# Optimization experiments

Hardware: AMD Instinct MI355X
Metric: run time of the kernel (lower is better)

The kernel has to match this reference:

```python
import jax, jax.numpy as jnp
import numpy as np

F_REP = 256
F_BET = 512
N_PER = 6
MAGNITUDE = 0.001


def _glorot(key, shape):
    fan_in = shape[0]
    return jax.random.normal(key, shape, dtype=jnp.float32) / np.sqrt(fan_in)


def setup_inputs() -> dict:
    key = jax.random.key(0)
    ks = jax.random.split(key, 24)
    n_atoms, n_tors = 50000, 300000
    inp = {
        'h': jax.random.normal(ks[0], (n_atoms, F_REP), dtype=jnp.float32),
        'idxs': jax.random.randint(ks[1], (n_tors, 4), 0, n_atoms, dtype=jnp.int64),
        # symmetrizer: skippedLinear(4*rep, bet) + DenseBlock(bet, depth=3)
        'Ws0': _glorot(ks[2], (4 * F_REP, F_BET)), 'bs0': jnp.zeros((F_BET,), jnp.float32),
        'Ws1': _glorot(ks[3], (F_BET, F_BET)), 'bs1': jnp.zeros((F_BET,), jnp.float32),
        'Ws2': _glorot(ks[4], (F_BET, F_BET)), 'bs2': jnp.zeros((F_BET,), jnp.float32),
        'Ws3': _glorot(ks[5], (F_BET, F_BET)), 'bs3': jnp.zeros((F_BET,), jnp.float32),
        # torsion_nn: DenseBlock(bet, depth=2) + Linear(bet, n_periodicity)
        'Wt0': _glorot(ks[6], (F_BET, F_BET)), 'bt0': jnp.zeros((F_BET,), jnp.float32),
        'Wt1': _glorot(ks[7], (F_BET, F_BET)), 'bt1': jnp.zeros((F_BET,), jnp.float32),
        'Wt2': _glorot(ks[8], (F_BET, N_PER)), 'bt2': jnp.zeros((N_PER,), jnp.float32),
        # classification_nn: skippedLinear(bet, bet) + Linear(bet, n_periodicity)
        'Wc0': _glorot(ks[9], (F_BET, F_BET)), 'bc0': jnp.zeros((F_BET,), jnp.float32),
        'Wc1': _glorot(ks[10], (F_BET, N_PER)), 'bc1': jnp.zeros((N_PER,), jnp.float32),
    }
    return inp


def _symmetrizer(x, Ws0, bs0, Ws1, bs1, Ws2, bs2, Ws3, bs3):
    # skippedLinear(4*rep, bet): dims differ -> plain Linear + ELU
    h = jax.nn.elu(x @ Ws0 + bs0)
    # DenseBlock: residual Linear+ELU layers (in==out)
    for W, b in ((Ws1, bs1), (Ws2, bs2), (Ws3, bs3)):
        h = h + jax.nn.elu(h @ W + b)
    return h


def reference(h, idxs, Ws0, bs0, Ws1, bs1, Ws2, bs2, Ws3, bs3,
              Wt0, bt0, Wt1, bt1, Wt2, bt2, Wc0, bc0, Wc1, bc1):
    feats = h[idxs]  # [N, 4, F_REP] gather
    f1, f2, f3, f4 = feats[:, 0], feats[:, 1], feats[:, 2], feats[:, 3]
    x_fwd = jnp.concatenate([f1, f2, f3, f4], axis=-1)  # [N, 4F]
    x_rev = jnp.concatenate([f4, f3, f2, f1], axis=-1)
    sym = (_symmetrizer(x_fwd, Ws0, bs0, Ws1, bs1, Ws2, bs2, Ws3, bs3)
           + _symmetrizer(x_rev, Ws0, bs0, Ws1, bs1, Ws2, bs2, Ws3, bs3))
    # torsion_nn
    t = sym + jax.nn.elu(sym @ Wt0 + bt0)
    t = t + jax.nn.elu(t @ Wt1 + bt1)
    coeffs = t @ Wt2 + bt2  # [N, n_periodicity]
    # classification_nn (skippedLinear with in==out -> residual)
    c = sym + jax.nn.elu(sym @ Wc0 + bc0)
    score = c @ Wc1 + bc1  # [N, n_periodicity]
    gate = jax.nn.sigmoid(score)  # hardness == 1
    k = coeffs * MAGNITUDE * gate
    return jnp.stack([score, k])  # [2, N, n_periodicity]
```

## Files before the change

### kernel.cpp

```cpp
#include <hip/hip_runtime.h>

#define BM 64
#define NTHREADS 512
#define NT2 1024

typedef __attribute__((ext_vector_type(8))) short short8;
typedef __attribute__((ext_vector_type(4))) float f32x4;

__device__ __forceinline__ short f2bf(float f) {
  unsigned u = __builtin_bit_cast(unsigned, f);
  u += 0x7FFFu + ((u >> 16) & 1u);
  return (short)(u >> 16);
}
__device__ __forceinline__ float bf2f(short s) {
  unsigned u = ((unsigned)(unsigned short)s) << 16;
  return __builtin_bit_cast(float, u);
}
__device__ __forceinline__ float elu_f(float v) {
  return v > 0.f ? v : (__expf(v) - 1.f);
}

__global__ __launch_bounds__(256) void pack_w(const float* __restrict__ src,
                                              short* __restrict__ dst,
                                              int K, int N, int rev) {
  int tile = blockIdx.x * 4 + (threadIdx.x >> 6);
  int lane = threadIdx.x & 63;
  int ktiles = K >> 5;
  int tot = (N >> 4) * ktiles;
  if (tile >= tot) return;
  int nt = tile / ktiles, kt = tile - nt * ktiles;
  int col = (nt << 4) + (lane & 15);
  int k0 = (kt << 5) + ((lane >> 4) << 3);
  short8 o;
#pragma unroll
  for (int j = 0; j < 8; ++j) {
    int kr = k0 + j;
    if (rev) kr = ((3 - (kr >> 8)) << 8) | (kr & 255);
    o[j] = f2bf(src[(size_t)kr * N + col]);
  }
  *(short8*)(dst + (size_t)tile * 512 + lane * 8) = o;
}

__device__ __forceinline__ short8 lds_afrag(const char* base, int stride, int rt,
                                            int kt, int lane) {
  int row = rt * 16 + (lane & 15);
  int boff = (kt << 6) + ((lane >> 4) << 4);
  return *(const short8*)(base + row * stride + (boff ^ ((row & 7) << 4)));
}
__device__ __forceinline__ short8 ldg_bfrag(const short* W, int ktiles, int ct,
                                            int kt, int lane) {
  return *(const short8*)(W + ((size_t)(ct * ktiles + kt) << 9) + (lane << 3));
}

__global__ __launch_bounds__(NTHREADS) void atom_pre(const float* __restrict__ h,
                                                     const short* __restrict__ W0f,
                                                     short* __restrict__ p,
                                                     int n_atoms) {
  __shared__ char sh[BM * 512];
  const int tid = threadIdx.x, lane = tid & 63, wv = tid >> 6;
  const int r0 = blockIdx.x * BM;
  for (int i = tid; i < BM * 32; i += NTHREADS) {
    int row = i >> 5, c0 = (i & 31) << 3;
    int ga = r0 + row;
    short8 o;
    if (ga < n_atoms) {
      const float4* s4 = (const float4*)(h + (size_t)ga * 256 + c0);
      float4 v0 = s4[0], v1 = s4[1];
      o[0] = f2bf(v0.x); o[1] = f2bf(v0.y); o[2] = f2bf(v0.z); o[3] = f2bf(v0.w);
      o[4] = f2bf(v1.x); o[5] = f2bf(v1.y); o[6] = f2bf(v1.z); o[7] = f2bf(v1.w);
    } else {
#pragma unroll
      for (int e = 0; e < 8; ++e) o[e] = 0;
    }
    *(short8*)(sh + row * 512 + ((c0 * 2) ^ ((row & 7) << 4))) = o;
  }
  __syncthreads();
#pragma unroll 1
  for (int s = 0; s < 4; ++s) {
    f32x4 acc[4][4];
    const f32x4 z = {0.f, 0.f, 0.f, 0.f};
#pragma unroll
    for (int rt = 0; rt < 4; ++rt)
#pragma unroll
      for (int cf = 0; cf < 4; ++cf) acc[rt][cf] = z;
    for (int kt = 0; kt < 8; ++kt) {
      short8 a[4], b[4];
#pragma unroll
      for (int rt = 0; rt < 4; ++rt) a[rt] = lds_afrag(sh, 512, rt, kt, lane);
#pragma unroll
      for (int cf = 0; cf < 4; ++cf)
        b[cf] = ldg_bfrag(W0f, 32, (wv << 2) + cf, (s << 3) + kt, lane);
#pragma unroll
      for (int rt = 0; rt < 4; ++rt)
#pragma unroll
        for (int cf = 0; cf < 4; ++cf)
          acc[rt][cf] = __builtin_amdgcn_mfma_f32_16x16x32_bf16(a[rt], b[cf], acc[rt][cf], 0, 0, 0);
    }
#pragma unroll
    for (int rt = 0; rt < 4; ++rt)
#pragma unroll
      for (int cf = 0; cf < 4; ++cf) {
        int col = (wv << 6) + (cf << 4) + (lane & 15);
#pragma unroll
        for (int i = 0; i < 4; ++i) {
          int row = rt * 16 + ((lane >> 4) << 2) + i;
          int ga = r0 + row;
          if (ga < n_atoms) p[((size_t)ga * 4 + s) * 512 + col] = f2bf(acc[rt][cf][i]);
        }
      }
  }
}

struct P2 {
  const int* idxs;
  const short* p;
  const short *W1, *W2, *W3, *Wt0, *Wt1, *Wc0;
  const float *bs0, *bs1, *bs2, *bs3, *bt0, *bt1, *bt2, *bc0, *bc1;
  const float *Wt2, *Wc1;
  float* out;
  int n_tors;
};

template <bool SYM>
__device__ __forceinline__ void layer_dual3(char* hf, char* hr,
                                            const short* __restrict__ W,
                                            const float* __restrict__ bias,
                                            int wv, int lane) {
  f32x4 accf[4][2], accr[4][2];
  const f32x4 z = {0.f, 0.f, 0.f, 0.f};
#pragma unroll
  for (int rt = 0; rt < 4; ++rt)
#pragma unroll
    for (int cf = 0; cf < 2; ++cf) { accf[rt][cf] = z; accr[rt][cf] = z; }
  short8 bC[2], bN[2];
#pragma unroll
  for (int cf = 0; cf < 2; ++cf) bC[cf] = ldg_bfrag(W, 16, (wv << 1) + cf, 0, lane);
#pragma unroll 1
  for (int kt = 0; kt < 16; ++kt) {
#pragma unroll
    for (int cf = 0; cf < 2; ++cf)
      bN[cf] = ldg_bfrag(W, 16, (wv << 1) + cf, (kt + 1) & 15, lane);
    short8 af[4], ar[4];
#pragma unroll
    for (int rt = 0; rt < 4; ++rt) {
      af[rt] = lds_afrag(hf, 1024, rt, kt, lane);
      ar[rt] = lds_afrag(hr, 1024, rt, kt, lane);
    }
#pragma unroll
    for (int rt = 0; rt < 4; ++rt)
#pragma unroll
      for (int cf = 0; cf < 2; ++cf) {
        accf[rt][cf] = __builtin_amdgcn_mfma_f32_16x16x32_bf16(af[rt], bC[cf], accf[rt][cf], 0, 0, 0);
        accr[rt][cf] = __builtin_amdgcn_mfma_f32_16x16x32_bf16(ar[rt], bC[cf], accr[rt][cf], 0, 0, 0);
      }
#pragma unroll
    for (int cf = 0; cf < 2; ++cf) bC[cf] = bN[cf];
  }
  float bcol[2];
#pragma unroll
  for (int cf = 0; cf < 2; ++cf) bcol[cf] = bias[(wv << 5) + (cf << 4) + (lane & 15)];
  __syncthreads();
#pragma unroll
  for (int rt = 0; rt < 4; ++rt)
#pragma unroll
    for (int cf = 0; cf < 2; ++cf) {
      int col = (wv << 5) + (cf << 4) + (lane & 15);
#pragma unroll
      for (int i = 0; i < 4; ++i) {
        int row = rt * 16 + ((lane >> 4) << 2) + i;
        size_t off = (size_t)row * 1024 + ((col * 2) ^ ((row & 7) << 4));
        short* pf = (short*)(hf + off);
        short* pr = (short*)(hr + off);
        float nf = bf2f(*pf) + elu_f(accf[rt][cf][i] + bcol[cf]);
        float nr = bf2f(*pr) + elu_f(accr[rt][cf][i] + bcol[cf]);
        if (SYM) {
          *pf = f2bf(nf + nr);
        } else {
          *pf = f2bf(nf);
          *pr = f2bf(nr);
        }
      }
    }
  __syncthreads();
}

__device__ __forceinline__ void layer_single3(const char* in,
                                              const short* __restrict__ W,
                                              const float* __restrict__ bias,
                                              const char* res, char* out,
                                              int wv, int lane) {
  f32x4 acc[4][2];
  const f32x4 z = {0.f, 0.f, 0.f, 0.f};
#pragma unroll
  for (int rt = 0; rt < 4; ++rt)
#pragma unroll
    for (int cf = 0; cf < 2; ++cf) acc[rt][cf] = z;
  short8 bC[2], bN[2];
#pragma unroll
  for (int cf = 0; cf < 2; ++cf) bC[cf] = ldg_bfrag(W, 16, (wv << 1) + cf, 0, lane);
#pragma unroll 1
  for (int kt = 0; kt < 16; ++kt) {
#pragma unroll
    for (int cf = 0; cf < 2; ++cf)
      bN[cf] = ldg_bfrag(W, 16, (wv << 1) + cf, (kt + 1) & 15, lane);
    short8 a[4];
#pragma unroll
    for (int rt = 0; rt < 4; ++rt) a[rt] = lds_afrag(in, 1024, rt, kt, lane);
#pragma unroll
    for (int rt = 0; rt < 4; ++rt)
#pragma unroll
      for (int cf = 0; cf < 2; ++cf)
        acc[rt][cf] = __builtin_amdgcn_mfma_f32_16x16x32_bf16(a[rt], bC[cf], acc[rt][cf], 0, 0, 0);
#pragma unroll
    for (int cf = 0; cf < 2; ++cf) bC[cf] = bN[cf];
  }
  float bcol[2];
#pragma unroll
  for (int cf = 0; cf < 2; ++cf) bcol[cf] = bias[(wv << 5) + (cf << 4) + (lane & 15)];
  __syncthreads();
#pragma unroll
  for (int rt = 0; rt < 4; ++rt)
#pragma unroll
    for (int cf = 0; cf < 2; ++cf) {
      int col = (wv << 5) + (cf << 4) + (lane & 15);
#pragma unroll
      for (int i = 0; i < 4; ++i) {
        int row = rt * 16 + ((lane >> 4) << 2) + i;
        size_t off = (size_t)row * 1024 + ((col * 2) ^ ((row & 7) << 4));
        float v = elu_f(acc[rt][cf][i] + bcol[cf]) + bf2f(*(const short*)(res + off));
        *(short*)(out + off) = f2bf(v);
      }
    }
  __syncthreads();
}

__global__ __launch_bounds__(NT2) void fused2(P2 p) {
  __shared__ char smem[BM * 2048];
  __shared__ int sIdx[BM * 4];
  __shared__ float sSmall[BM * 12];
  char* sA = smem;
  char* sB = smem + BM * 1024;
  const int tid = threadIdx.x;
  const int lane = tid & 63;
  const int wv = tid >> 6;
  const int r0 = blockIdx.x * BM;

  for (int i = tid; i < BM * 4; i += NT2) {
    int grow = r0 + (i >> 2);
    sIdx[i] = (grow < p.n_tors) ? p.idxs[(size_t)grow * 4 + (i & 3)] : 0;
  }
  __syncthreads();

  for (int i = tid; i < BM * 64; i += NT2) {
    int row = i >> 6, c0 = (i & 63) << 3;
    float sf[8], sr[8];
#pragma unroll
    for (int e = 0; e < 8; ++e) { sf[e] = p.bs0[c0 + e]; sr[e] = sf[e]; }
#pragma unroll
    for (int j = 0; j < 4; ++j) {
      int a = sIdx[row * 4 + j];
      short8 vf = *(const short8*)(p.p + ((size_t)a * 4 + j) * 512 + c0);
      short8 vr = *(const short8*)(p.p + ((size_t)a * 4 + (3 - j)) * 512 + c0);
#pragma unroll
      for (int e = 0; e < 8; ++e) { sf[e] += bf2f(vf[e]); sr[e] += bf2f(vr[e]); }
    }
    short8 of, orv;
#pragma unroll
    for (int e = 0; e < 8; ++e) { of[e] = f2bf(elu_f(sf[e])); orv[e] = f2bf(elu_f(sr[e])); }
    size_t off = (size_t)row * 1024 + ((c0 * 2) ^ ((row & 7) << 4));
    *(short8*)(sA + off) = of;
    *(short8*)(sB + off) = orv;
  }
  __syncthreads();

  layer_dual3<false>(sA, sB, p.W1, p.bs1, wv, lane);
  layer_dual3<false>(sA, sB, p.W2, p.bs2, wv, lane);
  layer_dual3<true >(sA, sB, p.W3, p.bs3, wv, lane);

  layer_single3(sA, p.Wt0, p.bt0, sA, sB, wv, lane);
  layer_single3(sB, p.Wt1, p.bt1, sB, sB, wv, lane);
  layer_single3(sA, p.Wc0, p.bc0, sA, sA, wv, lane);

  for (int idx = tid; idx < BM * 12; idx += NT2) {
    int row = idx / 12, jj = idx - row * 12;
    int j = (jj < 6) ? jj : jj - 6;
    const char* src = (jj < 6) ? sB : sA;
    const float* W = (jj < 6) ? p.Wt2 : p.Wc1;
    float acc = (jj < 6) ? p.bt2[j] : p.bc1[j];
    for (int c0 = 0; c0 < 512; c0 += 8) {
      short8 v = *(const short8*)(src + (size_t)row * 1024 + ((c0 * 2) ^ ((row & 7) << 4)));
#pragma unroll
      for (int e = 0; e < 8; ++e) acc += bf2f(v[e]) * W[(c0 + e) * 6 + j];
    }
    sSmall[row * 12 + jj] = acc;
  }
  __syncthreads();
  for (int idx = tid; idx < BM * 6; idx += NT2) {
    int row = idx / 6, j = idx - row * 6;
    int grow = r0 + row;
    if (grow < p.n_tors) {
      float score = sSmall[row * 12 + 6 + j];
      float coeff = sSmall[row * 12 + j];
      p.out[(size_t)grow * 6 + j] = score;
      p.out[(size_t)p.n_tors * 6 + (size_t)grow * 6 + j] =
          coeff * 0.001f * (1.0f / (1.0f + __expf(-score)));
    }
  }
}


struct Params {
  const float* h;
  const int* idxs;
  const short *W0f, *W0r, *W1, *W2, *W3, *Wt0, *Wt1, *Wc0;
  const float *bs0, *bs1, *bs2, *bs3, *bt0, *bt1, *bt2, *bc0, *bc1;
  const float *Wt2, *Wc1;
  float* out;
  int n_tors;
};

__device__ __forceinline__ void layer_dual(char* hf, char* hr,
                                           const short* __restrict__ W,
                                           const float* __restrict__ bias,
                                           int wv, int lane) {
  f32x4 accf[4][4], accr[4][4];
  const f32x4 z = {0.f, 0.f, 0.f, 0.f};
#pragma unroll
  for (int rt = 0; rt < 4; ++rt)
#pragma unroll
    for (int cf = 0; cf < 4; ++cf) { accf[rt][cf] = z; accr[rt][cf] = z; }
  for (int kt = 0; kt < 16; ++kt) {
    short8 af[4], ar[4], b[4];
#pragma unroll
    for (int rt = 0; rt < 4; ++rt) {
      af[rt] = lds_afrag(hf, 1024, rt, kt, lane);
      ar[rt] = lds_afrag(hr, 1024, rt, kt, lane);
    }
#pragma unroll
    for (int cf = 0; cf < 4; ++cf) b[cf] = ldg_bfrag(W, 16, (wv << 2) + cf, kt, lane);
#pragma unroll
    for (int rt = 0; rt < 4; ++rt)
#pragma unroll
      for (int cf = 0; cf < 4; ++cf) {
        accf[rt][cf] = __builtin_amdgcn_mfma_f32_16x16x32_bf16(af[rt], b[cf], accf[rt][cf], 0, 0, 0);
        accr[rt][cf] = __builtin_amdgcn_mfma_f32_16x16x32_bf16(ar[rt], b[cf], accr[rt][cf], 0, 0, 0);
      }
  }
  float bcol[4];
#pragma unroll
  for (int cf = 0; cf < 4; ++cf) bcol[cf] = bias[(wv << 6) + (cf << 4) + (lane & 15)];
  __syncthreads();
#pragma unroll
  for (int rt = 0; rt < 4; ++rt)
#pragma unroll
    for (int cf = 0; cf < 4; ++cf) {
      int col = (wv << 6) + (cf << 4) + (lane & 15);
#pragma unroll
      for (int i = 0; i < 4; ++i) {
        int row = rt * 16 + ((lane >> 4) << 2) + i;
        size_t off = (size_t)row * 1024 + ((col * 2) ^ ((row & 7) << 4));
        short* pf = (short*)(hf + off);
        short* pr = (short*)(hr + off);
        *pf = f2bf(bf2f(*pf) + elu_f(accf[rt][cf][i] + bcol[cf]));
        *pr = f2bf(bf2f(*pr) + elu_f(accr[rt][cf][i] + bcol[cf]));
      }
    }
  __syncthreads();
}

__device__ __forceinline__ void layer_single(const char* in,
                                             const short* __restrict__ W,
                                             const float* __restrict__ bias,
                                             const char* res, char* out,
                                             int wv, int lane) {
  f32x4 acc[4][4];
  const f32x4 z = {0.f, 0.f, 0.f, 0.f};
#pragma unroll
  for (int rt = 0; rt < 4; ++rt)
#pragma unroll
    for (int cf = 0; cf < 4; ++cf) acc[rt][cf] = z;
  for (int kt = 0; kt < 16; ++kt) {
    short8 a[4], b[4];
#pragma unroll
    for (int rt = 0; rt < 4; ++rt) a[rt] = lds_afrag(in, 1024, rt, kt, lane);
#pragma unroll
    for (int cf = 0; cf < 4; ++cf) b[cf] = ldg_bfrag(W, 16, (wv << 2) + cf, kt, lane);
#pragma unroll
    for (int rt = 0; rt < 4; ++rt)
#pragma unroll
      for (int cf = 0; cf < 4; ++cf)
        acc[rt][cf] = __builtin_amdgcn_mfma_f32_16x16x32_bf16(a[rt], b[cf], acc[rt][cf], 0, 0, 0);
  }
  float bcol[4];
#pragma unroll
  for (int cf = 0; cf < 4; ++cf) bcol[cf] = bias[(wv << 6) + (cf << 4) + (lane & 15)];
  __syncthreads();
#pragma unroll
  for (int rt = 0; rt < 4; ++rt)
#pragma unroll
    for (int cf = 0; cf < 4; ++cf) {
      int col = (wv << 6) + (cf << 4) + (lane & 15);
#pragma unroll
      for (int i = 0; i < 4; ++i) {
        int row = rt * 16 + ((lane >> 4) << 2) + i;
        size_t off = (size_t)row * 1024 + ((col * 2) ^ ((row & 7) << 4));
        float v = elu_f(acc[rt][cf][i] + bcol[cf]) + bf2f(*(const short*)(res + off));
        *(short*)(out + off) = f2bf(v);
      }
    }
  __syncthreads();
}

__global__ __launch_bounds__(NTHREADS) void fused(Params p) {
  __shared__ char smem[BM * 2048];
  __shared__ float sSmall[BM * 12];
  char* sA = smem;
  char* sB = smem + BM * 1024;
  const int tid = threadIdx.x;
  const int lane = tid & 63;
  const int wv = tid >> 6;
  const int r0 = blockIdx.x * BM;

  for (int c = tid; c < BM * 128; c += NTHREADS) {
    int row = c >> 7;
    int col0 = (c & 127) << 3;
    int grow = r0 + row;
    short8 o;
    if (grow < p.n_tors) {
      int f = col0 >> 8;
      int cin = col0 & 255;
      int a = p.idxs[(size_t)grow * 4 + f];
      const float4* s4 = (const float4*)(p.h + (size_t)a * 256 + cin);
      float4 v0 = s4[0], v1 = s4[1];
      o[0] = f2bf(v0.x); o[1] = f2bf(v0.y); o[2] = f2bf(v0.z); o[3] = f2bf(v0.w);
      o[4] = f2bf(v1.x); o[5] = f2bf(v1.y); o[6] = f2bf(v1.z); o[7] = f2bf(v1.w);
    } else {
#pragma unroll
      for (int e = 0; e < 8; ++e) o[e] = 0;
    }
    *(short8*)(smem + (size_t)row * 2048 + ((col0 * 2) ^ ((row & 7) << 4))) = o;
  }
  __syncthreads();

  {
    f32x4 accf[4][4], accr[4][4];
    const f32x4 z = {0.f, 0.f, 0.f, 0.f};
#pragma unroll
    for (int rt = 0; rt < 4; ++rt)
#pragma unroll
      for (int cf = 0; cf < 4; ++cf) { accf[rt][cf] = z; accr[rt][cf] = z; }
    for (int kt = 0; kt < 32; ++kt) {
      short8 a[4], bfw[4], brw[4];
#pragma unroll
      for (int rt = 0; rt < 4; ++rt) a[rt] = lds_afrag(smem, 2048, rt, kt, lane);
#pragma unroll
      for (int cf = 0; cf < 4; ++cf) {
        bfw[cf] = ldg_bfrag(p.W0f, 32, (wv << 2) + cf, kt, lane);
        brw[cf] = ldg_bfrag(p.W0r, 32, (wv << 2) + cf, kt, lane);
      }
#pragma unroll
      for (int rt = 0; rt < 4; ++rt)
#pragma unroll
        for (int cf = 0; cf < 4; ++cf) {
          accf[rt][cf] = __builtin_amdgcn_mfma_f32_16x16x32_bf16(a[rt], bfw[cf], accf[rt][cf], 0, 0, 0);
          accr[rt][cf] = __builtin_amdgcn_mfma_f32_16x16x32_bf16(a[rt], brw[cf], accr[rt][cf], 0, 0, 0);
        }
    }
    float bcol[4];
#pragma unroll
    for (int cf = 0; cf < 4; ++cf) bcol[cf] = p.bs0[(wv << 6) + (cf << 4) + (lane & 15)];
    __syncthreads();
#pragma unroll
    for (int rt = 0; rt < 4; ++rt)
#pragma unroll
      for (int cf = 0; cf < 4; ++cf) {
        int col = (wv << 6) + (cf << 4) + (lane & 15);
#pragma unroll
        for (int i = 0; i < 4; ++i) {
          int row = rt * 16 + ((lane >> 4) << 2) + i;
          size_t off = (size_t)row * 1024 + ((col * 2) ^ ((row & 7) << 4));
          *(short*)(sA + off) = f2bf(elu_f(accf[rt][cf][i] + bcol[cf]));
          *(short*)(sB + off) = f2bf(elu_f(accr[rt][cf][i] + bcol[cf]));
        }
      }
    __syncthreads();
  }

  layer_dual(sA, sB, p.W1, p.bs1, wv, lane);
  layer_dual(sA, sB, p.W2, p.bs2, wv, lane);
  layer_dual(sA, sB, p.W3, p.bs3, wv, lane);

  for (int c = tid; c < BM * 64; c += NTHREADS) {
    int row = c >> 6;
    int col0 = (c & 63) << 3;
    size_t off = (size_t)row * 1024 + ((col0 * 2) ^ ((row & 7) << 4));
    short8 xa = *(short8*)(sA + off);
    short8 xb = *(short8*)(sB + off);
    short8 o;
#pragma unroll
    for (int e = 0; e < 8; ++e) o[e] = f2bf(bf2f(xa[e]) + bf2f(xb[e]));
    *(short8*)(sA + off) = o;
  }
  __syncthreads();

  layer_single(sA, p.Wt0, p.bt0, sA, sB, wv, lane);
  layer_single(sB, p.Wt1, p.bt1, sB, sB, wv, lane);
  layer_single(sA, p.Wc0, p.bc0, sA, sA, wv, lane);

  for (int idx = tid; idx < BM * 12; idx += NTHREADS) {
    int row = idx / 12, jj = idx - row * 12;
    int j = (jj < 6) ? jj : jj - 6;
    const char* src = (jj < 6) ? sB : sA;
    const float* W = (jj < 6) ? p.Wt2 : p.Wc1;
    float acc = (jj < 6) ? p.bt2[j] : p.bc1[j];
    for (int c0 = 0; c0 < 512; c0 += 8) {
      short8 v = *(const short8*)(src + (size_t)row * 1024 + ((c0 * 2) ^ ((row & 7) << 4)));
#pragma unroll
      for (int e = 0; e < 8; ++e) acc += bf2f(v[e]) * W[(c0 + e) * 6 + j];
    }
    sSmall[row * 12 + jj] = acc;
  }
  __syncthreads();
  for (int idx = tid; idx < BM * 6; idx += NTHREADS) {
    int row = idx / 6, j = idx - row * 6;
    int grow = r0 + row;
    if (grow < p.n_tors) {
      float score = sSmall[row * 12 + 6 + j];
      float coeff = sSmall[row * 12 + j];
      p.out[(size_t)grow * 6 + j] = score;
      p.out[(size_t)p.n_tors * 6 + (size_t)grow * 6 + j] =
          coeff * 0.001f * (1.0f / (1.0f + __expf(-score)));
    }
  }
}


extern "C" void kernel_launch(void* const* d_in, const int* in_sizes, int n_in,
                              void* d_out, int out_size, void* d_ws, size_t ws_size,
                              hipStream_t stream) {
  const float* h   = (const float*)d_in[0];
  const int* idxs  = (const int*)d_in[1];
  const float* Ws0 = (const float*)d_in[2];
  const float* bs0 = (const float*)d_in[3];
  const float* Ws1 = (const float*)d_in[4];
  const float* bs1 = (const float*)d_in[5];
  const float* Ws2 = (const float*)d_in[6];
  const float* bs2 = (const float*)d_in[7];
  const float* Ws3 = (const float*)d_in[8];
  const float* bs3 = (const float*)d_in[9];
  const float* Wt0 = (const float*)d_in[10];
  const float* bt0 = (const float*)d_in[11];
  const float* Wt1 = (const float*)d_in[12];
  const float* bt1 = (const float*)d_in[13];
  const float* Wt2 = (const float*)d_in[14];
  const float* bt2 = (const float*)d_in[15];
  const float* Wc0 = (const float*)d_in[16];
  const float* bc0 = (const float*)d_in[17];
  const float* Wc1 = (const float*)d_in[18];
  const float* bc1 = (const float*)d_in[19];
  int n_tors = in_sizes[1] / 4;
  int n_atoms = in_sizes[0] / 256;

  auto pk = [&](const float* s, short* dmem, int K, int N, int rev) {
    int tiles = (N >> 4) * (K >> 5);
    pack_w<<<dim3((tiles + 3) / 4), dim3(256), 0, stream>>>(s, dmem, K, N, rev);
  };

  size_t pElems = (size_t)n_atoms * 4 * 512;
  size_t needNew = (pElems + 524288 + 6 * 262144) * sizeof(short);

  if (ws_size >= needNew) {
    short* ws = (short*)d_ws;
    short* pT  = ws;
    short* W0f = ws + pElems;
    short* W1  = W0f + 524288;
    short* W2  = W1 + 262144;
    short* W3  = W2 + 262144;
    short* Wt0c = W3 + 262144;
    short* Wt1c = Wt0c + 262144;
    short* Wc0c = Wt1c + 262144;

    pk(Ws0, W0f, 1024, 512, 0);
    pk(Ws1, W1, 512, 512, 0);
    pk(Ws2, W2, 512, 512, 0);
    pk(Ws3, W3, 512, 512, 0);
    pk(Wt0, Wt0c, 512, 512, 0);
    pk(Wt1, Wt1c, 512, 512, 0);
    pk(Wc0, Wc0c, 512, 512, 0);

    atom_pre<<<dim3((n_atoms + BM - 1) / BM), dim3(NTHREADS), 0, stream>>>(h, W0f, pT, n_atoms);

    P2 p;
    p.idxs = idxs; p.p = pT;
    p.W1 = W1; p.W2 = W2; p.W3 = W3;
    p.Wt0 = Wt0c; p.Wt1 = Wt1c; p.Wc0 = Wc0c;
    p.bs0 = bs0; p.bs1 = bs1; p.bs2 = bs2; p.bs3 = bs3;
    p.bt0 = bt0; p.bt1 = bt1; p.bt2 = bt2; p.bc0 = bc0; p.bc1 = bc1;
    p.Wt2 = Wt2; p.Wc1 = Wc1;
    p.out = (float*)d_out; p.n_tors = n_tors;

    fused2<<<dim3((n_tors + BM - 1) / BM), dim3(NT2), 0, stream>>>(p);
  } else {
    short* ws = (short*)d_ws;
    short* W0f = ws;
    short* W0r = ws + 524288;
    short* W1  = ws + 1048576;
    short* W2  = W1 + 262144;
    short* W3  = W2 + 262144;
    short* Wt0c = W3 + 262144;
    short* Wt1c = Wt0c + 262144;
    short* Wc0c = Wt1c + 262144;

    pk(Ws0, W0f, 1024, 512, 0);
    pk(Ws0, W0r, 1024, 512, 1);
    pk(Ws1, W1, 512, 512, 0);
    pk(Ws2, W2, 512, 512, 0);
    pk(Ws3, W3, 512, 512, 0);
    pk(Wt0, Wt0c, 512, 512, 0);
    pk(Wt1, Wt1c, 512, 512, 0);
    pk(Wc0, Wc0c, 512, 512, 0);

    Params p;
    p.h = h; p.idxs = idxs;
    p.W0f = W0f; p.W0r = W0r; p.W1 = W1; p.W2 = W2; p.W3 = W3;
    p.Wt0 = Wt0c; p.Wt1 = Wt1c; p.Wc0 = Wc0c;
    p.bs0 = bs0; p.bs1 = bs1; p.bs2 = bs2; p.bs3 = bs3;
    p.bt0 = bt0; p.bt1 = bt1; p.bt2 = bt2; p.bc0 = bc0; p.bc1 = bc1;
    p.Wt2 = Wt2; p.Wc1 = Wc1;
    p.out = (float*)d_out; p.n_tors = n_tors;

    fused<<<dim3((n_tors + BM - 1) / BM), dim3(NTHREADS), 0, stream>>>(p);
  }
}
```

Baseline: 3.191 ms.

## Split dual-stream layers into interleaved single-stream MFMA phases with fewer barriers

Replaces the dual forward/reverse layer (which held two accumulator sets and needed two barriers per layer) with single-stream MFMA phases that alternate between the forward and reverse buffers. Each phase's epilogue can overlap with the next phase's MFMA on the other buffer, using only one barrier between them. Bias is folded into the accumulator initialisation. The torsion and classification layers are reordered to fit the buffer usage. The aim is lower register pressure, since only one accumulator set is live in the MFMA loop, and fewer idle barrier stalls. The cost is that weight fragments are loaded from global memory twice per symmetrizer layer.

After: 3.227 ms. About the same (+1.1%).

```diff
diff --git a/kernel.cpp b/kernel.cpp
--- a/kernel.cpp
+++ b/kernel.cpp
@@ -121,17 +121,16 @@
   int n_tors;
 };
 
-template <bool SYM>
-__device__ __forceinline__ void layer_dual3(char* hf, char* hr,
-                                            const short* __restrict__ W,
-                                            const float* __restrict__ bias,
-                                            int wv, int lane) {
-  f32x4 accf[4][2], accr[4][2];
-  const f32x4 z = {0.f, 0.f, 0.f, 0.f};
-#pragma unroll
-  for (int rt = 0; rt < 4; ++rt)
-#pragma unroll
-    for (int cf = 0; cf < 2; ++cf) { accf[rt][cf] = z; accr[rt][cf] = z; }
+__device__ __forceinline__ void phase_mfma(const char* src, const short* __restrict__ W,
+                                           const float* __restrict__ bias,
+                                           f32x4 (&acc)[4][2], int wv, int lane) {
+  float b0 = bias[(wv << 5) + (lane & 15)];
+  float b1 = bias[(wv << 5) + 16 + (lane & 15)];
+#pragma unroll
+  for (int rt = 0; rt < 4; ++rt) {
+    acc[rt][0] = (f32x4){b0, b0, b0, b0};
+    acc[rt][1] = (f32x4){b1, b1, b1, b1};
+  }
   short8 bC[2], bN[2];
 #pragma unroll
   for (int cf = 0; cf < 2; ++cf) bC[cf] = ldg_bfrag(W, 16, (wv << 1) + cf, 0, lane);
@@ -140,26 +139,22 @@
 #pragma unroll
     for (int cf = 0; cf < 2; ++cf)
       bN[cf] = ldg_bfrag(W, 16, (wv << 1) + cf, (kt + 1) & 15, lane);
-    short8 af[4], ar[4];
-#pragma unroll
-    for (int rt = 0; rt < 4; ++rt) {
-      af[rt] = lds_afrag(hf, 1024, rt, kt, lane);
-      ar[rt] = lds_afrag(hr, 1024, rt, kt, lane);
-    }
-#pragma unroll
-    for (int rt = 0; rt < 4; ++rt)
-#pragma unroll
-      for (int cf = 0; cf < 2; ++cf) {
-        accf[rt][cf] = __builtin_amdgcn_mfma_f32_16x16x32_bf16(af[rt], bC[cf], accf[rt][cf], 0, 0, 0);
-        accr[rt][cf] = __builtin_amdgcn_mfma_f32_16x16x32_bf16(ar[rt], bC[cf], accr[rt][cf], 0, 0, 0);
-      }
+    short8 a[4];
+#pragma unroll
+    for (int rt = 0; rt < 4; ++rt) a[rt] = lds_afrag(src, 1024, rt, kt, lane);
+#pragma unroll
+    for (int rt = 0; rt < 4; ++rt)
+#pragma unroll
+      for (int cf = 0; cf < 2; ++cf)
+        acc[rt][cf] = __builtin_amdgcn_mfma_f32_16x16x32_bf16(a[rt], bC[cf], acc[rt][cf], 0, 0, 0);
 #pragma unroll
     for (int cf = 0; cf < 2; ++cf) bC[cf] = bN[cf];
   }
-  float bcol[2];
-#pragma unroll
-  for (int cf = 0; cf < 2; ++cf) bcol[cf] = bias[(wv << 5) + (cf << 4) + (lane & 15)];
-  __syncthreads();
+}
+
+template <bool EXTRA>
+__device__ __forceinline__ void epi_phase(char* dst, const char* res, const char* extra,
+                                          const f32x4 (&acc)[4][2], int wv, int lane) {
 #pragma unroll
   for (int rt = 0; rt < 4; ++rt)
 #pragma unroll
@@ -169,72 +164,14 @@
       for (int i = 0; i < 4; ++i) {
         int row = rt * 16 + ((lane >> 4) << 2) + i;
         size_t off = (size_t)row * 1024 + ((col * 2) ^ ((row & 7) << 4));
-        short* pf = (short*)(hf + off);
-        short* pr = (short*)(hr + off);
-        float nf = bf2f(*pf) + elu_f(accf[rt][cf][i] + bcol[cf]);
-        float nr = bf2f(*pr) + elu_f(accr[rt][cf][i] + bcol[cf]);
-        if (SYM) {
-          *pf = f2bf(nf + nr);
-        } else {
-          *pf = f2bf(nf);
-          *pr = f2bf(nr);
-        }
-      }
-    }
-  __syncthreads();
-}
-
-__device__ __forceinline__ void layer_single3(const char* in,
-                                              const short* __restrict__ W,
-                                              const float* __restrict__ bias,
-                                              const char* res, char* out,
-                                              int wv, int lane) {
-  f32x4 acc[4][2];
-  const f32x4 z = {0.f, 0.f, 0.f, 0.f};
-#pragma unroll
-  for (int rt = 0; rt < 4; ++rt)
-#pragma unroll
-    for (int cf = 0; cf < 2; ++cf) acc[rt][cf] = z;
-  short8 bC[2], bN[2];
-#pragma unroll
-  for (int cf = 0; cf < 2; ++cf) bC[cf] = ldg_bfrag(W, 16, (wv << 1) + cf, 0, lane);
-#pragma unroll 1
-  for (int kt = 0; kt < 16; ++kt) {
-#pragma unroll
-    for (int cf = 0; cf < 2; ++cf)
-      bN[cf] = ldg_bfrag(W, 16, (wv << 1) + cf, (kt + 1) & 15, lane);
-    short8 a[4];
-#pragma unroll
-    for (int rt = 0; rt < 4; ++rt) a[rt] = lds_afrag(in, 1024, rt, kt, lane);
-#pragma unroll
-    for (int rt = 0; rt < 4; ++rt)
-#pragma unroll
-      for (int cf = 0; cf < 2; ++cf)
-        acc[rt][cf] = __builtin_amdgcn_mfma_f32_16x16x32_bf16(a[rt], bC[cf], acc[rt][cf], 0, 0, 0);
-#pragma unroll
-    for (int cf = 0; cf < 2; ++cf) bC[cf] = bN[cf];
-  }
-  float bcol[2];
-#pragma unroll
-  for (int cf = 0; cf < 2; ++cf) bcol[cf] = bias[(wv << 5) + (cf << 4) + (lane & 15)];
-  __syncthreads();
-#pragma unroll
-  for (int rt = 0; rt < 4; ++rt)
-#pragma unroll
-    for (int cf = 0; cf < 2; ++cf) {
-      int col = (wv << 5) + (cf << 4) + (lane & 15);
-#pragma unroll
-      for (int i = 0; i < 4; ++i) {
-        int row = rt * 16 + ((lane >> 4) << 2) + i;
-        size_t off = (size_t)row * 1024 + ((col * 2) ^ ((row & 7) << 4));
-        float v = elu_f(acc[rt][cf][i] + bcol[cf]) + bf2f(*(const short*)(res + off));
-        *(short*)(out + off) = f2bf(v);
-      }
-    }
-  __syncthreads();
-}
-
-__global__ __launch_bounds__(NT2) void fused2(P2 p) {
+        float v = elu_f(acc[rt][cf][i]) + bf2f(*(const short*)(res + off));
+        if (EXTRA) v += bf2f(*(const short*)(extra + off));
+        *(short*)(dst + off) = f2bf(v);
+      }
+    }
+}
+
+__global__ __launch_bounds__(NT2) void fused3(P2 p) {
   __shared__ char smem[BM * 2048];
   __shared__ int sIdx[BM * 4];
   __shared__ float sSmall[BM * 12];
@@ -273,18 +210,42 @@
   }
   __syncthreads();
 
-  layer_dual3<false>(sA, sB, p.W1, p.bs1, wv, lane);
-  layer_dual3<false>(sA, sB, p.W2, p.bs2, wv, lane);
-  layer_dual3<true >(sA, sB, p.W3, p.bs3, wv, lane);
-
-  layer_single3(sA, p.Wt0, p.bt0, sA, sB, wv, lane);
-  layer_single3(sB, p.Wt1, p.bt1, sB, sB, wv, lane);
-  layer_single3(sA, p.Wc0, p.bc0, sA, sA, wv, lane);
+  f32x4 accA[4][2], accB[4][2];
+
+  phase_mfma(sA, p.W1, p.bs1, accA, wv, lane);
+  __syncthreads();
+  epi_phase<false>(sA, sA, nullptr, accA, wv, lane);
+  phase_mfma(sB, p.W1, p.bs1, accB, wv, lane);
+  __syncthreads();
+  epi_phase<false>(sB, sB, nullptr, accB, wv, lane);
+  phase_mfma(sA, p.W2, p.bs2, accA, wv, lane);
+  __syncthreads();
+  epi_phase<false>(sA, sA, nullptr, accA, wv, lane);
+  phase_mfma(sB, p.W2, p.bs2, accB, wv, lane);
+  __syncthreads();
+  epi_phase<false>(sB, sB, nullptr, accB, wv, lane);
+  phase_mfma(sA, p.W3, p.bs3, accA, wv, lane);
+  __syncthreads();
+  epi_phase<false>(sA, sA, nullptr, accA, wv, lane);
+  phase_mfma(sB, p.W3, p.bs3, accB, wv, lane);
+  __syncthreads();
+  epi_phase<true>(sB, sB, sA, accB, wv, lane);
+  __syncthreads();
+  phase_mfma(sB, p.Wt0, p.bt0, accA, wv, lane);
+  __syncthreads();
+  epi_phase<false>(sA, sB, nullptr, accA, wv, lane);
+  phase_mfma(sB, p.Wc0, p.bc0, accB, wv, lane);
+  __syncthreads();
+  epi_phase<false>(sB, sB, nullptr, accB, wv, lane);
+  phase_mfma(sA, p.Wt1, p.bt1, accA, wv, lane);
+  __syncthreads();
+  epi_phase<false>(sA, sA, nullptr, accA, wv, lane);
+  __syncthreads();
 
   for (int idx = tid; idx < BM * 12; idx += NT2) {
     int row = idx / 12, jj = idx - row * 12;
     int j = (jj < 6) ? jj : jj - 6;
-    const char* src = (jj < 6) ? sB : sA;
+    const char* src = (jj < 6) ? sA : sB;
     const float* W = (jj < 6) ? p.Wt2 : p.Wc1;
     float acc = (jj < 6) ? p.bt2[j] : p.bc1[j];
     for (int c0 = 0; c0 < 512; c0 += 8) {
@@ -599,7 +560,7 @@
     p.Wt2 = Wt2; p.Wc1 = Wc1;
     p.out = (float*)d_out; p.n_tors = n_tors;
 
-    fused2<<<dim3((n_tors + BM - 1) / BM), dim3(NT2), 0, stream>>>(p);
+    fused3<<<dim3((n_tors + BM - 1) / BM), dim3(NT2), 0, stream>>>(p);
   } else {
     short* ws = (short*)d_ws;
     short* W0f = ws;
```

## Shrink fused torsion kernel tile to 32 rows and merge Wt0/Wc0 GEMMs

Applied to the files above, without the earlier changes.

Replaces the 64-row fused kernel with a 32-row variant using 32KB of activation LDS, so more blocks can be resident per CU. Bias is folded into the accumulator initialisation. The Wt0 and Wc0 layers, which share the same input, now run as one pass that reads the A fragments once. The LDS swizzle gains an extra XOR bit to spread bank accesses. The cost is that each block of 32 rows streams the full weight set from global or L2, doubling weight traffic per row.

Measured after the change: 3.065 ms. 3.9% less time.

```diff
diff --git a/kernel.cpp b/kernel.cpp
--- a/kernel.cpp
+++ b/kernel.cpp
@@ -2,7 +2,8 @@
 
 #define BM 64
 #define NTHREADS 512
-#define NT2 1024
+#define BM4 32
+#define NT4 1024
 
 typedef __attribute__((ext_vector_type(8))) short short8;
 typedef __attribute__((ext_vector_type(4))) float f32x4;
@@ -41,15 +42,25 @@
   *(short8*)(dst + (size_t)tile * 512 + lane * 8) = o;
 }
 
-__device__ __forceinline__ short8 lds_afrag(const char* base, int stride, int rt,
+__device__ __forceinline__ short8 ldg_bfrag(const short* W, int ktiles, int ct,
                                             int kt, int lane) {
+  return *(const short8*)(W + ((size_t)(ct * ktiles + kt) << 9) + (lane << 3));
+}
+
+__device__ __forceinline__ int swz(int row, int boff) {
+  return row * 1024 + (boff ^ ((row & 7) << 4) ^ (((row >> 3) & 1) << 7));
+}
+__device__ __forceinline__ short8 lds_a32(const char* base, int rt, int kt, int lane) {
+  int row = rt * 16 + (lane & 15);
+  int boff = (kt << 6) + ((lane >> 4) << 4);
+  return *(const short8*)(base + swz(row, boff));
+}
+
+__device__ __forceinline__ short8 lds_afrag64(const char* base, int stride, int rt,
+                                              int kt, int lane) {
   int row = rt * 16 + (lane & 15);
   int boff = (kt << 6) + ((lane >> 4) << 4);
   return *(const short8*)(base + row * stride + (boff ^ ((row & 7) << 4)));
-}
-__device__ __forceinline__ short8 ldg_bfrag(const short* W, int ktiles, int ct,
-                                            int kt, int lane) {
-  return *(const short8*)(W + ((size_t)(ct * ktiles + kt) << 9) + (lane << 3));
 }
 
 __global__ __launch_bounds__(NTHREADS) void atom_pre(const float* __restrict__ h,
@@ -86,7 +97,7 @@
     for (int kt = 0; kt < 8; ++kt) {
       short8 a[4], b[4];
 #pragma unroll
-      for (int rt = 0; rt < 4; ++rt) a[rt] = lds_afrag(sh, 512, rt, kt, lane);
+      for (int rt = 0; rt < 4; ++rt) a[rt] = lds_afrag64(sh, 512, rt, kt, lane);
 #pragma unroll
       for (int cf = 0; cf < 4; ++cf)
         b[cf] = ldg_bfrag(W0f, 32, (wv << 2) + cf, (s << 3) + kt, lane);
@@ -121,17 +132,21 @@
   int n_tors;
 };
 
-template <bool SYM>
-__device__ __forceinline__ void layer_dual3(char* hf, char* hr,
-                                            const short* __restrict__ W,
-                                            const float* __restrict__ bias,
-                                            int wv, int lane) {
-  f32x4 accf[4][2], accr[4][2];
-  const f32x4 z = {0.f, 0.f, 0.f, 0.f};
-#pragma unroll
-  for (int rt = 0; rt < 4; ++rt)
-#pragma unroll
-    for (int cf = 0; cf < 2; ++cf) { accf[rt][cf] = z; accr[rt][cf] = z; }
+
+__device__ __forceinline__ void mfma_dual(const char* sA, const char* sB,
+                                          const short* __restrict__ W,
+                                          const float* __restrict__ bias,
+                                          f32x4 (&accf)[2][2], f32x4 (&accr)[2][2],
+                                          int wv, int lane) {
+  float b0 = bias[(wv << 5) + (lane & 15)];
+  float b1 = bias[(wv << 5) + 16 + (lane & 15)];
+#pragma unroll
+  for (int rt = 0; rt < 2; ++rt) {
+    accf[rt][0] = (f32x4){b0, b0, b0, b0};
+    accf[rt][1] = (f32x4){b1, b1, b1, b1};
+    accr[rt][0] = (f32x4){b0, b0, b0, b0};
+    accr[rt][1] = (f32x4){b1, b1, b1, b1};
+  }
   short8 bC[2], bN[2];
 #pragma unroll
   for (int cf = 0; cf < 2; ++cf) bC[cf] = ldg_bfrag(W, 16, (wv << 1) + cf, 0, lane);
@@ -140,61 +155,70 @@
 #pragma unroll
     for (int cf = 0; cf < 2; ++cf)
       bN[cf] = ldg_bfrag(W, 16, (wv << 1) + cf, (kt + 1) & 15, lane);
-    short8 af[4], ar[4];
-#pragma unroll
-    for (int rt = 0; rt < 4; ++rt) {
-      af[rt] = lds_afrag(hf, 1024, rt, kt, lane);
-      ar[rt] = lds_afrag(hr, 1024, rt, kt, lane);
-    }
-#pragma unroll
-    for (int rt = 0; rt < 4; ++rt)
+#pragma unroll
+    for (int rt = 0; rt < 2; ++rt) {
+      short8 af = lds_a32(sA, rt, kt, lane);
+      short8 ar = lds_a32(sB, rt, kt, lane);
 #pragma unroll
       for (int cf = 0; cf < 2; ++cf) {
-        accf[rt][cf] = __builtin_amdgcn_mfma_f32_16x16x32_bf16(af[rt], bC[cf], accf[rt][cf], 0, 0, 0);
-        accr[rt][cf] = __builtin_amdgcn_mfma_f32_16x16x32_bf16(ar[rt], bC[cf], accr[rt][cf], 0, 0, 0);
-      }
+        accf[rt][cf] = __builtin_amdgcn_mfma_f32_16x16x32_bf16(af, bC[cf], accf[rt][cf], 0, 0, 0);
+        accr[rt][cf] = __builtin_amdgcn_mfma_f32_16x16x32_bf16(ar, bC[cf], accr[rt][cf], 0, 0, 0);
+      }
+    }
 #pragma unroll
     for (int cf = 0; cf < 2; ++cf) bC[cf] = bN[cf];
   }
-  float bcol[2];
-#pragma unroll
-  for (int cf = 0; cf < 2; ++cf) bcol[cf] = bias[(wv << 5) + (cf << 4) + (lane & 15)];
-  __syncthreads();
-#pragma unroll
-  for (int rt = 0; rt < 4; ++rt)
+}
+
+__device__ __forceinline__ void mfma_dualB(const char* sA,
+                                           const short* __restrict__ Wa,
+                                           const short* __restrict__ Wb,
+                                           const float* __restrict__ ba,
+                                           const float* __restrict__ bb,
+                                           f32x4 (&accA)[2][2], f32x4 (&accB)[2][2],
+                                           int wv, int lane) {
+  float a0 = ba[(wv << 5) + (lane & 15)];
+  float a1 = ba[(wv << 5) + 16 + (lane & 15)];
+  float c0 = bb[(wv << 5) + (lane & 15)];
+  float c1 = bb[(wv << 5) + 16 + (lane & 15)];
+#pragma unroll
+  for (int rt = 0; rt < 2; ++rt) {
+    accA[rt][0] = (f32x4){a0, a0, a0, a0};
+    accA[rt][1] = (f32x4){a1, a1, a1, a1};
+    accB[rt][0] = (f32x4){c0, c0, c0, c0};
+    accB[rt][1] = (f32x4){c1, c1, c1, c1};
+  }
+#pragma unroll 1
+  for (int kt = 0; kt < 16; ++kt) {
+    short8 bA[2], bB[2];
 #pragma unroll
     for (int cf = 0; cf < 2; ++cf) {
-      int col = (wv << 5) + (cf << 4) + (lane & 15);
-#pragma unroll
-      for (int i = 0; i < 4; ++i) {
-        int row = rt * 16 + ((lane >> 4) << 2) + i;
-        size_t off = (size_t)row * 1024 + ((col * 2) ^ ((row & 7) << 4));
-        short* pf = (short*)(hf + off);
-        short* pr = (short*)(hr + off);
-        float nf = bf2f(*pf) + elu_f(accf[rt][cf][i] + bcol[cf]);
-        float nr = bf2f(*pr) + elu_f(accr[rt][cf][i] + bcol[cf]);
-        if (SYM) {
-          *pf = f2bf(nf + nr);
-        } else {
-          *pf = f2bf(nf);
-          *pr = f2bf(nr);
-        }
-      }
-    }
-  __syncthreads();
-}
-
-__device__ __forceinline__ void layer_single3(const char* in,
-                                              const short* __restrict__ W,
-                                              const float* __restrict__ bias,
-                                              const char* res, char* out,
-                                              int wv, int lane) {
-  f32x4 acc[4][2];
-  const f32x4 z = {0.f, 0.f, 0.f, 0.f};
-#pragma unroll
-  for (int rt = 0; rt < 4; ++rt)
-#pragma unroll
-    for (int cf = 0; cf < 2; ++cf) acc[rt][cf] = z;
+      bA[cf] = ldg_bfrag(Wa, 16, (wv << 1) + cf, kt, lane);
+      bB[cf] = ldg_bfrag(Wb, 16, (wv << 1) + cf, kt, lane);
+    }
+#pragma unroll
+    for (int rt = 0; rt < 2; ++rt) {
+      short8 a = lds_a32(sA, rt, kt, lane);
+#pragma unroll
+      for (int cf = 0; cf < 2; ++cf) {
+        accA[rt][cf] = __builtin_amdgcn_mfma_f32_16x16x32_bf16(a, bA[cf], accA[rt][cf], 0, 0, 0);
+        accB[rt][cf] = __builtin_amdgcn_mfma_f32_16x16x32_bf16(a, bB[cf], accB[rt][cf], 0, 0, 0);
+      }
+    }
+  }
+}
+
+__device__ __forceinline__ void mfma_single(const char* src,
+                                            const short* __restrict__ W,
+                                            const float* __restrict__ bias,
+                                            f32x4 (&acc)[2][2], int wv, int lane) {
+  float b0 = bias[(wv << 5) + (lane & 15)];
+  float b1 = bias[(wv << 5) + 16 + (lane & 15)];
+#pragma unroll
+  for (int rt = 0; rt < 2; ++rt) {
+    acc[rt][0] = (f32x4){b0, b0, b0, b0};
+    acc[rt][1] = (f32x4){b1, b1, b1, b1};
+  }
   short8 bC[2], bN[2];
 #pragma unroll
   for (int cf = 0; cf < 2; ++cf) bC[cf] = ldg_bfrag(W, 16, (wv << 1) + cf, 0, lane);
@@ -203,55 +227,36 @@
 #pragma unroll
     for (int cf = 0; cf < 2; ++cf)
       bN[cf] = ldg_bfrag(W, 16, (wv << 1) + cf, (kt + 1) & 15, lane);
-    short8 a[4];
-#pragma unroll
-    for (int rt = 0; rt < 4; ++rt) a[rt] = lds_afrag(in, 1024, rt, kt, lane);
-#pragma unroll
-    for (int rt = 0; rt < 4; ++rt)
+#pragma unroll
+    for (int rt = 0; rt < 2; ++rt) {
+      short8 a = lds_a32(src, rt, kt, lane);
 #pragma unroll
       for (int cf = 0; cf < 2; ++cf)
-        acc[rt][cf] = __builtin_amdgcn_mfma_f32_16x16x32_bf16(a[rt], bC[cf], acc[rt][cf], 0, 0, 0);
+        acc[rt][cf] = __builtin_amdgcn_mfma_f32_16x16x32_bf16(a, bC[cf], acc[rt][cf], 0, 0, 0);
+    }
 #pragma unroll
     for (int cf = 0; cf < 2; ++cf) bC[cf] = bN[cf];
   }
-  float bcol[2];
-#pragma unroll
-  for (int cf = 0; cf < 2; ++cf) bcol[cf] = bias[(wv << 5) + (cf << 4) + (lane & 15)];
-  __syncthreads();
-#pragma unroll
-  for (int rt = 0; rt < 4; ++rt)
-#pragma unroll
-    for (int cf = 0; cf < 2; ++cf) {
-      int col = (wv << 5) + (cf << 4) + (lane & 15);
-#pragma unroll
-      for (int i = 0; i < 4; ++i) {
-        int row = rt * 16 + ((lane >> 4) << 2) + i;
-        size_t off = (size_t)row * 1024 + ((col * 2) ^ ((row & 7) << 4));
-        float v = elu_f(acc[rt][cf][i] + bcol[cf]) + bf2f(*(const short*)(res + off));
-        *(short*)(out + off) = f2bf(v);
-      }
-    }
-  __syncthreads();
-}
-
-__global__ __launch_bounds__(NT2) void fused2(P2 p) {
-  __shared__ char smem[BM * 2048];
-  __shared__ int sIdx[BM * 4];
-  __shared__ float sSmall[BM * 12];
-  char* sA = smem;
-  char* sB = smem + BM * 1024;
+}
+
+__global__ __launch_bounds__(NT4, 8) void fused4(P2 p) {
+  __shared__ char sA[BM4 * 1024];
+  __shared__ char sB[BM4 * 1024];
+  __shared__ int sIdx[BM4 * 4];
+  __shared__ float sSmall[BM4 * 12];
   const int tid = threadIdx.x;
   const int lane = tid & 63;
   const int wv = tid >> 6;
-  const int r0 = blockIdx.x * BM;
-
-  for (int i = tid; i < BM * 4; i += NT2) {
-    int grow = r0 + (i >> 2);
-    sIdx[i] = (grow < p.n_tors) ? p.idxs[(size_t)grow * 4 + (i & 3)] : 0;
-  }
-  __syncthreads();
-
-  for (int i = tid; i < BM * 64; i += NT2) {
+  const int r0 = blockIdx.x * BM4;
+
+  if (tid < BM4 * 4) {
+    int grow = r0 + (tid >> 2);
+    sIdx[tid] = (grow < p.n_tors) ? p.idxs[(size_t)grow * 4 + (tid & 3)] : 0;
+  }
+  __syncthreads();
+
+#pragma unroll 1
+  for (int i = tid; i < BM4 * 64; i += NT4) {
     int row = i >> 6, c0 = (i & 63) << 3;
     float sf[8], sr[8];
 #pragma unroll
@@ -267,36 +272,96 @@
     short8 of, orv;
 #pragma unroll
     for (int e = 0; e < 8; ++e) { of[e] = f2bf(elu_f(sf[e])); orv[e] = f2bf(elu_f(sr[e])); }
-    size_t off = (size_t)row * 1024 + ((c0 * 2) ^ ((row & 7) << 4));
+    int off = swz(row, c0 * 2);
     *(short8*)(sA + off) = of;
     *(short8*)(sB + off) = orv;
   }
   __syncthreads();
 
-  layer_dual3<false>(sA, sB, p.W1, p.bs1, wv, lane);
-  layer_dual3<false>(sA, sB, p.W2, p.bs2, wv, lane);
-  layer_dual3<true >(sA, sB, p.W3, p.bs3, wv, lane);
-
-  layer_single3(sA, p.Wt0, p.bt0, sA, sB, wv, lane);
-  layer_single3(sB, p.Wt1, p.bt1, sB, sB, wv, lane);
-  layer_single3(sA, p.Wc0, p.bc0, sA, sA, wv, lane);
-
-  for (int idx = tid; idx < BM * 12; idx += NT2) {
-    int row = idx / 12, jj = idx - row * 12;
+  f32x4 accA[2][2], accB[2][2];
+
+  const short* Ws[3] = {p.W1, p.W2, p.W3};
+  const float* bs[3] = {p.bs1, p.bs2, p.bs3};
+#pragma unroll 1
+  for (int L = 0; L < 3; ++L) {
+    mfma_dual(sA, sB, Ws[L], bs[L], accA, accB, wv, lane);
+    __syncthreads();
+#pragma unroll
+    for (int rt = 0; rt < 2; ++rt)
+#pragma unroll
+      for (int cf = 0; cf < 2; ++cf) {
+        int col = (wv << 5) + (cf << 4) + (lane & 15);
+#pragma unroll
+        for (int i = 0; i < 4; ++i) {
+          int row = rt * 16 + ((lane >> 4) << 2) + i;
+          int off = swz(row, col * 2);
+          short* pf = (short*)(sA + off);
+          short* pr = (short*)(sB + off);
+          float nf = bf2f(*pf) + elu_f(accA[rt][cf][i]);
+          float nr = bf2f(*pr) + elu_f(accB[rt][cf][i]);
+          if (L == 2) {
+            *pf = f2bf(nf + nr);
+          } else {
+            *pf = f2bf(nf);
+            *pr = f2bf(nr);
+          }
+        }
+      }
+    __syncthreads();
+  }
+
+  mfma_dualB(sA, p.Wt0, p.Wc0, p.bt0, p.bc0, accA, accB, wv, lane);
+  __syncthreads();
+#pragma unroll
+  for (int rt = 0; rt < 2; ++rt)
+#pragma unroll
+    for (int cf = 0; cf < 2; ++cf) {
+      int col = (wv << 5) + (cf << 4) + (lane & 15);
+#pragma unroll
+      for (int i = 0; i < 4; ++i) {
+        int row = rt * 16 + ((lane >> 4) << 2) + i;
+        int off = swz(row, col * 2);
+        float s = bf2f(*(short*)(sA + off));
+        *(short*)(sB + off) = f2bf(s + elu_f(accA[rt][cf][i]));
+        *(short*)(sA + off) = f2bf(s + elu_f(accB[rt][cf][i]));
+      }
+    }
+  __syncthreads();
+
+  mfma_single(sB, p.Wt1, p.bt1, accA, wv, lane);
+  __syncthreads();
+#pragma unroll
+  for (int rt = 0; rt < 2; ++rt)
+#pragma unroll
+    for (int cf = 0; cf < 2; ++cf) {
+      int col = (wv << 5) + (cf << 4) + (lane & 15);
+#pragma unroll
+      for (int i = 0; i < 4; ++i) {
+        int row = rt * 16 + ((lane >> 4) << 2) + i;
+        int off = swz(row, col * 2);
+        short* pt = (short*)(sB + off);
+        *pt = f2bf(bf2f(*pt) + elu_f(accA[rt][cf][i]));
+      }
+    }
+  __syncthreads();
+
+  if (tid < BM4 * 12) {
+    int row = tid / 12, jj = tid - row * 12;
     int j = (jj < 6) ? jj : jj - 6;
     const char* src = (jj < 6) ? sB : sA;
     const float* W = (jj < 6) ? p.Wt2 : p.Wc1;
     float acc = (jj < 6) ? p.bt2[j] : p.bc1[j];
+#pragma unroll 1
     for (int c0 = 0; c0 < 512; c0 += 8) {
-      short8 v = *(const short8*)(src + (size_t)row * 1024 + ((c0 * 2) ^ ((row & 7) << 4)));
+      short8 v = *(const short8*)(src + swz(row, c0 * 2));
 #pragma unroll
       for (int e = 0; e < 8; ++e) acc += bf2f(v[e]) * W[(c0 + e) * 6 + j];
     }
     sSmall[row * 12 + jj] = acc;
   }
   __syncthreads();
-  for (int idx = tid; idx < BM * 6; idx += NT2) {
-    int row = idx / 6, j = idx - row * 6;
+  if (tid < BM4 * 6) {
+    int row = tid / 6, j = tid - row * 6;
     int grow = r0 + row;
     if (grow < p.n_tors) {
       float score = sSmall[row * 12 + 6 + j];
@@ -333,8 +398,8 @@
     short8 af[4], ar[4], b[4];
 #pragma unroll
     for (int rt = 0; rt < 4; ++rt) {
-      af[rt] = lds_afrag(hf, 1024, rt, kt, lane);
-      ar[rt] = lds_afrag(hr, 1024, rt, kt, lane);
+      af[rt] = lds_afrag64(hf, 1024, rt, kt, lane);
+      ar[rt] = lds_afrag64(hr, 1024, rt, kt, lane);
     }
 #pragma unroll
     for (int cf = 0; cf < 4; ++cf) b[cf] = ldg_bfrag(W, 16, (wv << 2) + cf, kt, lane);
@@ -382,7 +447,7 @@
   for (int kt = 0; kt < 16; ++kt) {
     short8 a[4], b[4];
 #pragma unroll
-    for (int rt = 0; rt < 4; ++rt) a[rt] = lds_afrag(in, 1024, rt, kt, lane);
+    for (int rt = 0; rt < 4; ++rt) a[rt] = lds_afrag64(in, 1024, rt, kt, lane);
 #pragma unroll
     for (int cf = 0; cf < 4; ++cf) b[cf] = ldg_bfrag(W, 16, (wv << 2) + cf, kt, lane);
 #pragma unroll
@@ -452,7 +517,7 @@
     for (int kt = 0; kt < 32; ++kt) {
       short8 a[4], bfw[4], brw[4];
 #pragma unroll
-      for (int rt = 0; rt < 4; ++rt) a[rt] = lds_afrag(smem, 2048, rt, kt, lane);
+      for (int rt = 0; rt < 4; ++rt) a[rt] = lds_afrag64(smem, 2048, rt, kt, lane);
 #pragma unroll
       for (int cf = 0; cf < 4; ++cf) {
         bfw[cf] = ldg_bfrag(p.W0f, 32, (wv << 2) + cf, kt, lane);
@@ -599,7 +664,7 @@
     p.Wt2 = Wt2; p.Wc1 = Wc1;
     p.out = (float*)d_out; p.n_tors = n_tors;
 
-    fused2<<<dim3((n_tors + BM - 1) / BM), dim3(NT2), 0, stream>>>(p);
+    fused4<<<dim3((n_tors + BM4 - 1) / BM4), dim3(NT4), 0, stream>>>(p);
   } else {
     short* ws = (short*)d_ws;
     short* W0f = ws;
```
